# Kernel optimization log

Measured on AMD Instinct MI355X. Metric: run time of the kernel, lower is better.

## Reference

```python
import jax, jax.numpy as jnp
import numpy as np
from jax import lax

EPSILON = 0.01
CLAMP_MIN = 0.8
CLAMP_MAX = 1.2


def setup_inputs() -> dict:
    key = jax.random.key(0)
    k1, k2, k3, k4 = jax.random.split(key, 4)
    B, T, D = 8, 4096, 1024
    write_signal = jax.random.normal(k1, (B, T, D), dtype=jnp.float32)
    pad_mask = jax.random.randint(k2, (B, T), 0, 2) == 1
    update_mask = jax.random.randint(k3, (B, T), 0, 2) == 1
    # trust_proj weight (dim -> 1, no bias); scaled small for a varied tanh regime
    w = jax.random.normal(k4, (D,), dtype=jnp.float32) * 0.02
    return {"write_signal": write_signal, "pad_mask": pad_mask,
            "update_mask": update_mask, "w": w}


def reference(write_signal, pad_mask, update_mask, w):
    # write_signal: (B, T, D); pad_mask/update_mask: (B, T) bool; w: (D,)
    B, T, D = write_signal.shape
    dtype = write_signal.dtype
    # gate_t = (~pad) * update, per the torch code's multiplied float masks
    gate = ((~pad_mask) & update_mask).astype(dtype)  # (B, T)

    def step(mem, inp):
        x_t, g_t = inp                      # x_t: (B, D), g_t: (B,)
        g = g_t[:, None]
        mem = (1.0 - EPSILON * g) * mem + EPSILON * x_t * g
        bias = 1.0 + jnp.tanh(mem @ w)      # (B,)
        return mem, bias

    xs = (jnp.swapaxes(write_signal, 0, 1), gate.T)  # time-major
    mem0 = jnp.zeros((B, D), dtype=dtype)
    memory, biases = lax.scan(step, mem0, xs)        # biases: (T, B)
    bias_stack = biases.T                            # (B, T)
    bias_stack = jnp.where(pad_mask, jnp.asarray(1.0, dtype), bias_stack)
    bias_stack = jnp.clip(bias_stack, CLAMP_MIN, CLAMP_MAX)
    return bias_stack, memory
```

## Files before the change

kernel.cpp:

```cpp
#include <hip/hip_runtime.h>

#define EPS 0.01f
#define B_ 8
#define T_ 4096
#define D_ 1024

#define TCHUNK 128
#define NBLK_T (T_ / TCHUNK)
__global__ __launch_bounds__(1024) void main_pass_kernel(
    const float* __restrict__ x, const float* __restrict__ w,
    const int* __restrict__ pad, const int* __restrict__ upd,
    float* __restrict__ y, float* __restrict__ mem_part) {
    const int b = blockIdx.y;
    const int tbase = blockIdx.x * TCHUNK;
    const int tid = threadIdx.x;
    const int wave = tid >> 6;
    const int lane = tid & 63;
    const int base = b * T_;

    __shared__ float alpha_s[TCHUNK];
    __shared__ int wtot[16];
    {
        const int4 pv = reinterpret_cast<const int4*>(pad + base)[tid];
        const int4 uv = reinterpret_cast<const int4*>(upd + base)[tid];
        int g[4];
        g[0] = (pv.x == 0 && uv.x != 0) ? 1 : 0;
        g[1] = (pv.y == 0 && uv.y != 0) ? 1 : 0;
        g[2] = (pv.z == 0 && uv.z != 0) ? 1 : 0;
        g[3] = (pv.w == 0 && uv.w != 0) ? 1 : 0;
        const int cnt = g[0] + g[1] + g[2] + g[3];

        int inc = cnt;
        #pragma unroll
        for (int off = 1; off <= 32; off <<= 1) {
            int n = __shfl_up(inc, off);
            if (lane >= off) inc += n;
        }
        if (lane == 63) wtot[wave] = inc;
        __syncthreads();
        if (wave == 0 && lane < 16) {
            int iv = wtot[lane];
            #pragma unroll
            for (int off = 1; off <= 8; off <<= 1) {
                int n = __shfl_up(iv, off);
                if (lane >= off) iv += n;
            }
            wtot[lane] = iv;
        }
        __syncthreads();
        const int total = wtot[15];
        int c = (wave > 0 ? wtot[wave - 1] : 0) + inc - cnt;

        const float L = -0.014499569695115089f;
        #pragma unroll
        for (int i = 0; i < 4; ++i) {
            const int t = 4 * tid + i;
            c += g[i];
            if (t >= tbase && t < tbase + TCHUNK)
                alpha_s[t - tbase] = g[i] ? EPS * exp2f((float)(total - c) * L) : 0.f;
        }
    }
    __syncthreads();

    float4 wv[4];
    #pragma unroll
    for (int k = 0; k < 4; ++k)
        wv[k] = *reinterpret_cast<const float4*>(w + k * 256 + lane * 4);

    float4 acc[4];
    #pragma unroll
    for (int k = 0; k < 4; ++k) acc[k] = make_float4(0.f, 0.f, 0.f, 0.f);

    for (int r = wave; r < TCHUNK; r += 16) {
        const float al = alpha_s[r];
        const int t = tbase + r;
        const float* rowp = x + ((size_t)b * T_ + t) * D_;
        if (al != 0.f) {
            float dot = 0.f;
            #pragma unroll
            for (int k = 0; k < 4; ++k) {
                float4 v = *reinterpret_cast<const float4*>(rowp + k * 256 + lane * 4);
                dot += v.x * wv[k].x + v.y * wv[k].y + v.z * wv[k].z + v.w * wv[k].w;
                acc[k].x += al * v.x;
                acc[k].y += al * v.y;
                acc[k].z += al * v.z;
                acc[k].w += al * v.w;
            }
            #pragma unroll
            for (int off = 32; off >= 1; off >>= 1)
                dot += __shfl_xor(dot, off);
            if (lane == 0) y[b * T_ + t] = dot;
        }
    }

    __shared__ float part[16][D_];
    #pragma unroll
    for (int k = 0; k < 4; ++k)
        *reinterpret_cast<float4*>(&part[wave][k * 256 + lane * 4]) = acc[k];
    __syncthreads();
    float sum = 0.f;
    #pragma unroll
    for (int w2 = 0; w2 < 16; ++w2) sum += part[w2][tid];
    mem_part[((size_t)b * NBLK_T + blockIdx.x) * D_ + tid] = sum;
}

__global__ __launch_bounds__(1024) void finalize_kernel(
    const float* __restrict__ y, const int* __restrict__ pad,
    const int* __restrict__ upd, const float* __restrict__ mem_part,
    float* __restrict__ bias, float* __restrict__ mem) {
    if (blockIdx.x >= B_) {
        const int b = blockIdx.x - B_;
        const int d = threadIdx.x;
        float sum = 0.f;
        #pragma unroll
        for (int i = 0; i < NBLK_T; ++i)
            sum += mem_part[((size_t)b * NBLK_T + i) * D_ + d];
        mem[b * D_ + d] = sum;
        return;
    }

    const int b = blockIdx.x;
    const int tid = threadIdx.x;
    const int wave = tid >> 6;
    const int lane = tid & 63;
    const int base = b * T_;

    const int4 pv = reinterpret_cast<const int4*>(pad + base)[tid];
    const int4 uv = reinterpret_cast<const int4*>(upd + base)[tid];
    const float4 yv = reinterpret_cast<const float4*>(y + base)[tid];
    int g[4];
    g[0] = (pv.x == 0 && uv.x != 0) ? 1 : 0;
    g[1] = (pv.y == 0 && uv.y != 0) ? 1 : 0;
    g[2] = (pv.z == 0 && uv.z != 0) ? 1 : 0;
    g[3] = (pv.w == 0 && uv.w != 0) ? 1 : 0;
    const float yl[4] = {yv.x, yv.y, yv.z, yv.w};

    float av[4], uvv[4];
    float a_c = 1.f, u_c = 0.f;
    #pragma unroll
    for (int i = 0; i < 4; ++i) {
        float a = g[i] ? (1.f - EPS) : 1.f;
        float u = g[i] ? EPS * yl[i] : 0.f;
        av[i] = a; uvv[i] = u;
        u_c = a * u_c + u;
        a_c = a * a_c;
    }

    float A = a_c, U = u_c;
    #pragma unroll
    for (int off = 1; off <= 32; off <<= 1) {
        float A1 = __shfl_up(A, off);
        float U1 = __shfl_up(U, off);
        if (lane >= off) { U = A * U1 + U; A = A * A1; }
    }
    __shared__ float wA[16], wU[16];
    if (lane == 63) { wA[wave] = A; wU[wave] = U; }
    __syncthreads();
    if (wave == 0 && lane < 16) {
        float A2 = wA[lane], U2 = wU[lane];
        #pragma unroll
        for (int off = 1; off <= 8; off <<= 1) {
            float A1 = __shfl_up(A2, off);
            float U1 = __shfl_up(U2, off);
            if (lane >= off) { U2 = A2 * U1 + U2; A2 = A2 * A1; }
        }
        wA[lane] = A2; wU[lane] = U2;
    }
    __syncthreads();
    float At = __shfl_up(A, 1), Ut = __shfl_up(U, 1);
    if (lane == 0) { At = 1.f; Ut = 0.f; }
    const float Uw = (wave > 0) ? wU[wave - 1] : 0.f;
    float s = At * Uw + Ut;

    const int pl[4] = {pv.x, pv.y, pv.z, pv.w};
    float4 bv;
    float* bp = &bv.x;
    #pragma unroll
    for (int i = 0; i < 4; ++i) {
        s = av[i] * s + uvv[i];
        float bval;
        if (pl[i] != 0) {
            bval = 1.f;
        } else {
            bval = 1.f + tanhf(s);
            bval = fminf(fmaxf(bval, 0.8f), 1.2f);
        }
        bp[i] = bval;
    }
    reinterpret_cast<float4*>(bias + base)[tid] = bv;
}

extern "C" void kernel_launch(void* const* d_in, const int* in_sizes, int n_in,
                              void* d_out, int out_size, void* d_ws, size_t ws_size,
                              hipStream_t stream) {
    const float* x  = (const float*)d_in[0];
    const int* pad  = (const int*)d_in[1];
    const int* upd  = (const int*)d_in[2];
    const float* w  = (const float*)d_in[3];

    float* out  = (float*)d_out;
    float* bias = out;
    float* mem  = out + B_ * T_;

    float* y        = (float*)d_ws;
    float* mem_part = y + B_ * T_;

    dim3 gridA(NBLK_T, B_);
    main_pass_kernel<<<gridA, 1024, 0, stream>>>(x, w, pad, upd, y, mem_part);
    finalize_kernel<<<2 * B_, 1024, 0, stream>>>(y, pad, upd, mem_part, bias, mem);
}
```

Before: 181.3 us.

## Fuse main pass and finalize into one kernel using release/acquire flags

Merges the two launches into a single kernel. Producer blocks publish partial sums and dot products, then set a per-block flag with a release store. Consumer blocks, placed after all producers in the grid, spin with acquire loads until their batch's flags are set, then run the scan and reduction. This removes the second launch and the gap between kernels, but relies on consumers not starving producers of residency. The flags are never reset, so a stale magic value left from an earlier call could let consumers read partial data before it is written.

```diff
diff --git a/kernel.cpp b/kernel.cpp
--- a/kernel.cpp
+++ b/kernel.cpp
@@ -4,113 +4,139 @@
 #define B_ 8
 #define T_ 4096
 #define D_ 1024
-
 #define TCHUNK 128
 #define NBLK_T (T_ / TCHUNK)
-__global__ __launch_bounds__(1024) void main_pass_kernel(
+#define NPROD (B_ * NBLK_T)
+#define FLAG_MAGIC 0x7F3A2B1Cu
+
+__global__ __launch_bounds__(1024) void fused_kernel(
     const float* __restrict__ x, const float* __restrict__ w,
     const int* __restrict__ pad, const int* __restrict__ upd,
-    float* __restrict__ y, float* __restrict__ mem_part) {
-    const int b = blockIdx.y;
-    const int tbase = blockIdx.x * TCHUNK;
+    float* __restrict__ y, float* __restrict__ mem_part,
+    unsigned* __restrict__ flags,
+    float* __restrict__ bias, float* __restrict__ mem) {
+    const int blk = blockIdx.x;
     const int tid = threadIdx.x;
     const int wave = tid >> 6;
     const int lane = tid & 63;
-    const int base = b * T_;
-
-    __shared__ float alpha_s[TCHUNK];
-    __shared__ int wtot[16];
-    {
-        const int4 pv = reinterpret_cast<const int4*>(pad + base)[tid];
-        const int4 uv = reinterpret_cast<const int4*>(upd + base)[tid];
-        int g[4];
-        g[0] = (pv.x == 0 && uv.x != 0) ? 1 : 0;
-        g[1] = (pv.y == 0 && uv.y != 0) ? 1 : 0;
-        g[2] = (pv.z == 0 && uv.z != 0) ? 1 : 0;
-        g[3] = (pv.w == 0 && uv.w != 0) ? 1 : 0;
-        const int cnt = g[0] + g[1] + g[2] + g[3];
-
-        int inc = cnt;
-        #pragma unroll
-        for (int off = 1; off <= 32; off <<= 1) {
-            int n = __shfl_up(inc, off);
-            if (lane >= off) inc += n;
-        }
-        if (lane == 63) wtot[wave] = inc;
+
+    if (blk < NPROD) {
+        const int b = blk >> 5;
+        const int bx = blk & 31;
+        const int tbase = bx * TCHUNK;
+        const int base = b * T_;
+
+        __shared__ float alpha_s[TCHUNK];
+        __shared__ int wtot[16];
+        {
+            const int4 pv = reinterpret_cast<const int4*>(pad + base)[tid];
+            const int4 uv = reinterpret_cast<const int4*>(upd + base)[tid];
+            int g[4];
+            g[0] = (pv.x == 0 && uv.x != 0) ? 1 : 0;
+            g[1] = (pv.y == 0 && uv.y != 0) ? 1 : 0;
+            g[2] = (pv.z == 0 && uv.z != 0) ? 1 : 0;
+            g[3] = (pv.w == 0 && uv.w != 0) ? 1 : 0;
+            const int cnt = g[0] + g[1] + g[2] + g[3];
+
+            int inc = cnt;
+            #pragma unroll
+            for (int off = 1; off <= 32; off <<= 1) {
+                int n = __shfl_up(inc, off);
+                if (lane >= off) inc += n;
+            }
+            if (lane == 63) wtot[wave] = inc;
+            __syncthreads();
+            if (wave == 0 && lane < 16) {
+                int iv = wtot[lane];
+                #pragma unroll
+                for (int off = 1; off <= 8; off <<= 1) {
+                    int n = __shfl_up(iv, off);
+                    if (lane >= off) iv += n;
+                }
+                wtot[lane] = iv;
+            }
+            __syncthreads();
+            const int total = wtot[15];
+            int c = (wave > 0 ? wtot[wave - 1] : 0) + inc - cnt;
+            const float L = -0.014499569695115089f;
+            #pragma unroll
+            for (int i = 0; i < 4; ++i) {
+                const int t = 4 * tid + i;
+                c += g[i];
+                if (t >= tbase && t < tbase + TCHUNK)
+                    alpha_s[t - tbase] = g[i] ? EPS * exp2f((float)(total - c) * L) : 0.f;
+            }
+        }
         __syncthreads();
-        if (wave == 0 && lane < 16) {
-            int iv = wtot[lane];
-            #pragma unroll
-            for (int off = 1; off <= 8; off <<= 1) {
-                int n = __shfl_up(iv, off);
-                if (lane >= off) iv += n;
-            }
-            wtot[lane] = iv;
-        }
+
+        float4 wv[4];
+        #pragma unroll
+        for (int k = 0; k < 4; ++k)
+            wv[k] = *reinterpret_cast<const float4*>(w + k * 256 + lane * 4);
+
+        float4 acc[4];
+        #pragma unroll
+        for (int k = 0; k < 4; ++k) acc[k] = make_float4(0.f, 0.f, 0.f, 0.f);
+
+        for (int r = wave; r < TCHUNK; r += 16) {
+            const float al = alpha_s[r];
+            const int t = tbase + r;
+            const float* rowp = x + ((size_t)b * T_ + t) * D_;
+            if (al != 0.f) {
+                float dot = 0.f;
+                #pragma unroll
+                for (int k = 0; k < 4; ++k) {
+                    float4 v = *reinterpret_cast<const float4*>(rowp + k * 256 + lane * 4);
+                    dot += v.x * wv[k].x + v.y * wv[k].y + v.z * wv[k].z + v.w * wv[k].w;
+                    acc[k].x += al * v.x;
+                    acc[k].y += al * v.y;
+                    acc[k].z += al * v.z;
+                    acc[k].w += al * v.w;
+                }
+                #pragma unroll
+                for (int off = 32; off >= 1; off >>= 1)
+                    dot += __shfl_xor(dot, off);
+                if (lane == 0) y[b * T_ + t] = dot;
+            }
+        }
+
+        __shared__ float part[16][D_];
+        #pragma unroll
+        for (int k = 0; k < 4; ++k)
+            *reinterpret_cast<float4*>(&part[wave][k * 256 + lane * 4]) = acc[k];
         __syncthreads();
-        const int total = wtot[15];
-        int c = (wave > 0 ? wtot[wave - 1] : 0) + inc - cnt;
-
-        const float L = -0.014499569695115089f;
-        #pragma unroll
-        for (int i = 0; i < 4; ++i) {
-            const int t = 4 * tid + i;
-            c += g[i];
-            if (t >= tbase && t < tbase + TCHUNK)
-                alpha_s[t - tbase] = g[i] ? EPS * exp2f((float)(total - c) * L) : 0.f;
+        float sum = 0.f;
+        #pragma unroll
+        for (int w2 = 0; w2 < 16; ++w2) sum += part[w2][tid];
+        mem_part[((size_t)b * NBLK_T + bx) * D_ + tid] = sum;
+
+        __threadfence();
+        __syncthreads();
+        if (tid == 0)
+            __hip_atomic_store(&flags[blk], FLAG_MAGIC, __ATOMIC_RELEASE,
+                               __HIP_MEMORY_SCOPE_AGENT);
+        return;
+    }
+
+    const int role = blk - NPROD;
+    const int b = role & 7;
+
+    if (wave == 0) {
+        bool done = false;
+        while (!done) {
+            unsigned v = FLAG_MAGIC;
+            if (lane < NBLK_T)
+                v = __hip_atomic_load(&flags[b * NBLK_T + lane], __ATOMIC_ACQUIRE,
+                                      __HIP_MEMORY_SCOPE_AGENT);
+            done = __all(v == FLAG_MAGIC);
+            if (!done) __builtin_amdgcn_s_sleep(8);
         }
     }
     __syncthreads();
-
-    float4 wv[4];
-    #pragma unroll
-    for (int k = 0; k < 4; ++k)
-        wv[k] = *reinterpret_cast<const float4*>(w + k * 256 + lane * 4);
-
-    float4 acc[4];
-    #pragma unroll
-    for (int k = 0; k < 4; ++k) acc[k] = make_float4(0.f, 0.f, 0.f, 0.f);
-
-    for (int r = wave; r < TCHUNK; r += 16) {
-        const float al = alpha_s[r];
-        const int t = tbase + r;
-        const float* rowp = x + ((size_t)b * T_ + t) * D_;
-        if (al != 0.f) {
-            float dot = 0.f;
-            #pragma unroll
-            for (int k = 0; k < 4; ++k) {
-                float4 v = *reinterpret_cast<const float4*>(rowp + k * 256 + lane * 4);
-                dot += v.x * wv[k].x + v.y * wv[k].y + v.z * wv[k].z + v.w * wv[k].w;
-                acc[k].x += al * v.x;
-                acc[k].y += al * v.y;
-                acc[k].z += al * v.z;
-                acc[k].w += al * v.w;
-            }
-            #pragma unroll
-            for (int off = 32; off >= 1; off >>= 1)
-                dot += __shfl_xor(dot, off);
-            if (lane == 0) y[b * T_ + t] = dot;
-        }
-    }
-
-    __shared__ float part[16][D_];
-    #pragma unroll
-    for (int k = 0; k < 4; ++k)
-        *reinterpret_cast<float4*>(&part[wave][k * 256 + lane * 4]) = acc[k];
-    __syncthreads();
-    float sum = 0.f;
-    #pragma unroll
-    for (int w2 = 0; w2 < 16; ++w2) sum += part[w2][tid];
-    mem_part[((size_t)b * NBLK_T + blockIdx.x) * D_ + tid] = sum;
-}
-
-__global__ __launch_bounds__(1024) void finalize_kernel(
-    const float* __restrict__ y, const int* __restrict__ pad,
-    const int* __restrict__ upd, const float* __restrict__ mem_part,
-    float* __restrict__ bias, float* __restrict__ mem) {
-    if (blockIdx.x >= B_) {
-        const int b = blockIdx.x - B_;
-        const int d = threadIdx.x;
+    __threadfence();
+
+    if (role >= B_) {
+        const int d = tid;
         float sum = 0.f;
         #pragma unroll
         for (int i = 0; i < NBLK_T; ++i)
@@ -119,12 +145,7 @@
         return;
     }
 
-    const int b = blockIdx.x;
-    const int tid = threadIdx.x;
-    const int wave = tid >> 6;
-    const int lane = tid & 63;
     const int base = b * T_;
-
     const int4 pv = reinterpret_cast<const int4*>(pad + base)[tid];
     const int4 uv = reinterpret_cast<const int4*>(upd + base)[tid];
     const float4 yv = reinterpret_cast<const float4*>(y + base)[tid];
@@ -204,8 +225,8 @@
 
     float* y        = (float*)d_ws;
     float* mem_part = y + B_ * T_;
-
-    dim3 gridA(NBLK_T, B_);
-    main_pass_kernel<<<gridA, 1024, 0, stream>>>(x, w, pad, upd, y, mem_part);
-    finalize_kernel<<<2 * B_, 1024, 0, stream>>>(y, pad, upd, mem_part, bias, mem);
+    unsigned* flags = (unsigned*)(mem_part + (size_t)B_ * NBLK_T * D_);
+
+    fused_kernel<<<NPROD + 2 * B_, 1024, 0, stream>>>(
+        x, w, pad, upd, y, mem_part, flags, bias, mem);
 }
```

Result: slower. 257.5 us (+42.0%).
